# Kernel tuning notes

Hardware: AMD Instinct MI355X
Metric: run time of the kernel (lower is better)

## Reference

```python
import jax, jax.numpy as jnp
import numpy as np


def setup_inputs() -> dict:
    key = jax.random.key(0)
    ks = jax.random.split(key, 9)
    B, Nq, Nkv, C, ICO = 1, 512, 2562, 64, 64
    return {
        "q": jax.random.normal(ks[0], (B, Nq, C), jnp.float32),
        "q_coord": jax.random.normal(ks[1], (B, Nq, 3), jnp.float32),
        "kv": jax.random.normal(ks[2], (B, Nkv, ICO), jnp.float32),
        "kv_coord": jax.random.normal(ks[3], (B, Nkv, 3), jnp.float32),
        "Wq": jax.random.normal(ks[4], (C, C), jnp.float32) * (C ** -0.5),
        "Wkv": jax.random.normal(ks[5], (ICO, 2 * C), jnp.float32) * (ICO ** -0.5),
        "Wdelta": jax.random.normal(ks[6], (3, C), jnp.float32) * (3 ** -0.5),
        "Wproj": jax.random.normal(ks[7], (C, C), jnp.float32) * (C ** -0.5),
        "bproj": jnp.zeros((C,), jnp.float32),
    }


def reference(q, q_coord, kv, kv_coord, Wq, Wkv, Wdelta, Wproj, bproj):
    C = q.shape[-1]
    scale = 1.0 / C  # erp_dim ** -1 (qk_scale=None)
    q_ = q @ Wq                                   # [B, Nq, C]
    kv_ = kv @ Wkv                                # [B, Nkv, 2C]
    k, v = jnp.split(kv_, 2, axis=-1)             # each [B, Nkv, C]
    # positional encoding: exp(-|dq - dk|) over 3D coords, projected to C
    pos_enc = jnp.exp(-jnp.abs(q_coord[:, :, None] - kv_coord[:, None])) @ Wdelta  # [B,Nq,Nkv,C]
    # elementwise abs-diff attention score, reduced over channel dim
    score = (jnp.exp(-jnp.abs(q_[:, :, None] - k[:, None])) + pos_enc).sum(-1) * scale  # [B,Nq,Nkv]
    attn = jax.nn.softmax(score, axis=-1)
    out = attn @ v                                # [B, Nq, C]
    return out @ Wproj + bproj
```

## Files before the change

### kernel.cpp

```cpp
#include <hip/hip_runtime.h>

#define NQ   512
#define NKV  2562
#define CH   64
#define QB   2
#define BT   512
#define NJQ  4
#define JQ   641
#define PSTRIDE 132
#define LOG2E 1.44269504088896340736f

#define KVROWS 8
#define NKVB ((NKV + KVROWS - 1) / KVROWS)
#define QROWS 16
#define NQB (NQ / QROWS)
#define NCB  41

static __device__ __forceinline__ float exp2_raw(float x) {
  float r; asm("v_exp_f32 %0, %1" : "=v"(r) : "v"(x)); return r;
}
static __device__ __forceinline__ float exp2_negabs(float x) {
  float r; asm("v_exp_f32 %0, -abs(%1)" : "=v"(r) : "v"(x)); return r;
}
#define E2(a, b) exp2_negabs((a) - (b))

__global__ __launch_bounds__(256) void gemm_qkv(
    const float* __restrict__ q, const float* __restrict__ kv,
    const float* __restrict__ Wq, const float* __restrict__ Wkv,
    const float* __restrict__ kvc, float* __restrict__ qp,
    float* __restrict__ kvp, float* __restrict__ kvc4) {
  const int tid = threadIdx.x;
  if (blockIdx.x < NKVB) {
    const int j0 = blockIdx.x * KVROWS;
    __shared__ float s_in[KVROWS][CH];
    if (tid < KVROWS * (CH / 4)) {
      int r = tid >> 4, g = tid & 15;
      int j = j0 + r;
      float4 v = (j < NKV) ? ((const float4*)(kv + (size_t)j * CH))[g]
                           : make_float4(0.f, 0.f, 0.f, 0.f);
      ((float4*)&s_in[r][0])[g] = v;
    }
    __syncthreads();
    const int r = tid >> 5;
    const int mg = (tid & 31) * 4;
    float4 acc = make_float4(0.f, 0.f, 0.f, 0.f);
#pragma unroll 16
    for (int rr = 0; rr < CH; ++rr) {
      float a = s_in[r][rr];
      float4 w = *(const float4*)(Wkv + (size_t)rr * 2 * CH + mg);
      acc.x = fmaf(a, w.x, acc.x); acc.y = fmaf(a, w.y, acc.y);
      acc.z = fmaf(a, w.z, acc.z); acc.w = fmaf(a, w.w, acc.w);
    }
    if (mg < CH) {
      acc.x *= LOG2E; acc.y *= LOG2E; acc.z *= LOG2E; acc.w *= LOG2E;
    }
    int j = j0 + r;
    if (j < NKV) *(float4*)(kvp + (size_t)j * 2 * CH + mg) = acc;
  } else if (blockIdx.x < NKVB + NQB) {
    const int i0 = (blockIdx.x - NKVB) * QROWS;
    __shared__ float s_in[QROWS][CH];
    {
      int r = tid >> 4, g = tid & 15;
      float4 v = ((const float4*)(q + (size_t)(i0 + r) * CH))[g];
      ((float4*)&s_in[r][0])[g] = v;
    }
    __syncthreads();
    const int r = tid >> 4;
    const int cg = (tid & 15) * 4;
    float4 acc = make_float4(0.f, 0.f, 0.f, 0.f);
#pragma unroll 16
    for (int rr = 0; rr < CH; ++rr) {
      float a = s_in[r][rr];
      float4 w = *(const float4*)(Wq + (size_t)rr * CH + cg);
      acc.x = fmaf(a, w.x, acc.x); acc.y = fmaf(a, w.y, acc.y);
      acc.z = fmaf(a, w.z, acc.z); acc.w = fmaf(a, w.w, acc.w);
    }
    acc.x *= LOG2E; acc.y *= LOG2E; acc.z *= LOG2E; acc.w *= LOG2E;
    *(float4*)(qp + (size_t)(i0 + r) * CH + cg) = acc;
  } else {
    int t = (blockIdx.x - NKVB - NQB) * 256 + tid;
    if (t < NKV * 4) {
      int j = t >> 2, d = t & 3;
      kvc4[t] = (d < 3) ? kvc[(size_t)j * 3 + d] * LOG2E : 0.f;
    }
  }
}

__global__ __launch_bounds__(BT, 4) void attn_part(
    const float* __restrict__ qp, const float* __restrict__ kvp,
    const float* __restrict__ qc, const float* __restrict__ kvc4,
    const float* __restrict__ Wdelta, float* __restrict__ part) {
  __shared__ float s_score[QB][JQ];
  __shared__ float s_red[QB][BT];
  __shared__ float s_wd[3];

  const int qpair = blockIdx.x >> 2;
  const int h = blockIdx.x & 3;
  const int i0 = qpair * QB;
  const int jlo = h * JQ;
  const int jhi = (jlo + JQ < NKV) ? jlo + JQ : NKV;

  const int tid = threadIdx.x;
  const int sub = tid & 3;
  const int c0 = sub * 16;
  const int wid = tid >> 6;
  const int lane = tid & 63;

  if (tid < 3) {
    float s = 0.f;
    for (int c = 0; c < CH; ++c) s += Wdelta[tid * CH + c];
    s_wd[tid] = s;
  }

  const float4* q0p = (const float4*)(qp + (size_t)i0 * CH + c0);
  const float4* q1p = (const float4*)(qp + (size_t)(i0 + 1) * CH + c0);
  float4 qa0 = q0p[0], qa1 = q0p[1], qa2 = q0p[2], qa3 = q0p[3];
  float4 qb0 = q1p[0], qb1 = q1p[1], qb2 = q1p[2], qb3 = q1p[3];
  asm volatile("" : "+v"(qa0.x), "+v"(qa0.y), "+v"(qa0.z), "+v"(qa0.w),
                    "+v"(qa1.x), "+v"(qa1.y), "+v"(qa1.z), "+v"(qa1.w),
                    "+v"(qa2.x), "+v"(qa2.y), "+v"(qa2.z), "+v"(qa2.w),
                    "+v"(qa3.x), "+v"(qa3.y), "+v"(qa3.z), "+v"(qa3.w));
  asm volatile("" : "+v"(qb0.x), "+v"(qb0.y), "+v"(qb0.z), "+v"(qb0.w),
                    "+v"(qb1.x), "+v"(qb1.y), "+v"(qb1.z), "+v"(qb1.w),
                    "+v"(qb2.x), "+v"(qb2.y), "+v"(qb2.z), "+v"(qb2.w),
                    "+v"(qb3.x), "+v"(qb3.y), "+v"(qb3.z), "+v"(qb3.w));

  float qc0[3], qc1[3];
#pragma unroll
  for (int d = 0; d < 3; ++d) {
    qc0[d] = qc[(size_t)i0 * 3 + d] * LOG2E;
    qc1[d] = qc[(size_t)(i0 + 1) * 3 + d] * LOG2E;
  }
  __syncthreads();
  const float wd0 = s_wd[0], wd1 = s_wd[1], wd2 = s_wd[2];
  const float pscale = (1.0f / 64.0f) * LOG2E;

  const int step = BT / 4;
  float ls0 = 0.f, ls1 = 0.f;
  int j = jlo + (tid >> 2);
  float4 k0, k1, k2, k3, cc;
  {
    int jc = (j < jhi) ? j : jlo;
    const float4* kr = (const float4*)(kvp + (size_t)jc * 128 + c0);
    k0 = kr[0]; k1 = kr[1]; k2 = kr[2]; k3 = kr[3];
    cc = *(const float4*)(kvc4 + (size_t)jc * 4);
  }
  while (j < jhi) {
    const int jn = j + step;
    const int jnc = (jn < jhi) ? jn : jlo;
    const float4* krn = (const float4*)(kvp + (size_t)jnc * 128 + c0);
    float4 n0 = krn[0], n1 = krn[1], n2 = krn[2], n3 = krn[3];
    float4 cn = *(const float4*)(kvc4 + (size_t)jnc * 4);

    float s0 = ((E2(qa0.x, k0.x) + E2(qa0.y, k0.y)) + (E2(qa0.z, k0.z) + E2(qa0.w, k0.w)))
             + ((E2(qa1.x, k1.x) + E2(qa1.y, k1.y)) + (E2(qa1.z, k1.z) + E2(qa1.w, k1.w)))
             + ((E2(qa2.x, k2.x) + E2(qa2.y, k2.y)) + (E2(qa2.z, k2.z) + E2(qa2.w, k2.w)))
             + ((E2(qa3.x, k3.x) + E2(qa3.y, k3.y)) + (E2(qa3.z, k3.z) + E2(qa3.w, k3.w)));
    float s1 = ((E2(qb0.x, k0.x) + E2(qb0.y, k0.y)) + (E2(qb0.z, k0.z) + E2(qb0.w, k0.w)))
             + ((E2(qb1.x, k1.x) + E2(qb1.y, k1.y)) + (E2(qb1.z, k1.z) + E2(qb1.w, k1.w)))
             + ((E2(qb2.x, k2.x) + E2(qb2.y, k2.y)) + (E2(qb2.z, k2.z) + E2(qb2.w, k2.w)))
             + ((E2(qb3.x, k3.x) + E2(qb3.y, k3.y)) + (E2(qb3.z, k3.z) + E2(qb3.w, k3.w)));
    s0 += __shfl_xor(s0, 1); s0 += __shfl_xor(s0, 2);
    s1 += __shfl_xor(s1, 1); s1 += __shfl_xor(s1, 2);
    if (sub == 0) {
      s0 += E2(qc0[0], cc.x) * wd0 + E2(qc0[1], cc.y) * wd1 + E2(qc0[2], cc.z) * wd2;
      s1 += E2(qc1[0], cc.x) * wd0 + E2(qc1[1], cc.y) * wd1 + E2(qc1[2], cc.z) * wd2;
      float p0 = exp2_raw(s0 * pscale);
      float p1 = exp2_raw(s1 * pscale);
      s_score[0][j - jlo] = p0; s_score[1][j - jlo] = p1;
      ls0 += p0; ls1 += p1;
    }
    k0 = n0; k1 = n1; k2 = n2; k3 = n3; cc = cn;
    j = jn;
  }

#pragma unroll
  for (int off = 1; off < 64; off <<= 1) {
    ls0 += __shfl_xor(ls0, off);
    ls1 += __shfl_xor(ls1, off);
  }
  if (lane == 0) { s_red[0][wid] = ls0; s_red[1][wid] = ls1; }
  __syncthreads();
  float t0 = s_red[0][0], t1 = s_red[1][0];
#pragma unroll
  for (int w = 1; w < BT / 64; ++w) { t0 += s_red[0][w]; t1 += s_red[1][w]; }
  __syncthreads();

  const int c = tid & 63, g = tid >> 6;
  float a0 = 0.f, a1 = 0.f;
#pragma unroll 8
  for (int j2 = jlo + g; j2 < jhi; j2 += 8) {
    float v = kvp[(size_t)j2 * 128 + 64 + c];
    a0 = fmaf(s_score[0][j2 - jlo], v, a0);
    a1 = fmaf(s_score[1][j2 - jlo], v, a1);
  }
  s_red[0][tid] = a0; s_red[1][tid] = a1;
  __syncthreads();

  float* P = part + (size_t)(qpair * NJQ + h) * PSTRIDE;
  if (g == 0) {
    float u0 = 0.f, u1 = 0.f;
#pragma unroll
    for (int gg = 0; gg < 8; ++gg) {
      u0 += s_red[0][gg * 64 + c];
      u1 += s_red[1][gg * 64 + c];
    }
    P[4 + c] = u0;
    P[68 + c] = u1;
    if (c == 0) { P[0] = t0; P[1] = t1; }
  }
}

__global__ __launch_bounds__(256) void attn_merge(
    const float* __restrict__ part, const float* __restrict__ Wproj,
    const float* __restrict__ bproj, float* __restrict__ out) {
  __shared__ float s_o[4][CH];
  const int tid = threadIdx.x;
  const int g = tid >> 6, c = tid & 63;
  const int i = blockIdx.x * 4 + g;
  const int qpi = i >> 1, qs = i & 1;

  float ssum = 0.f, osum = 0.f;
#pragma unroll
  for (int h = 0; h < NJQ; ++h) {
    const float* P = part + (size_t)(qpi * NJQ + h) * PSTRIDE;
    ssum += P[qs];
    osum += P[4 + qs * 64 + c];
  }
  s_o[g][c] = osum / ssum;
  __syncthreads();

  float acc = 0.f;
#pragma unroll 16
  for (int r = 0; r < CH; ++r)
    acc = fmaf(s_o[g][r], Wproj[r * CH + c], acc);
  out[(size_t)i * CH + c] = acc + bproj[c];
}

extern "C" void kernel_launch(void* const* d_in, const int* in_sizes, int n_in,
                              void* d_out, int out_size, void* d_ws, size_t ws_size,
                              hipStream_t stream) {
  const float* q      = (const float*)d_in[0];
  const float* qc     = (const float*)d_in[1];
  const float* kv     = (const float*)d_in[2];
  const float* kvc    = (const float*)d_in[3];
  const float* Wq     = (const float*)d_in[4];
  const float* Wkv    = (const float*)d_in[5];
  const float* Wdelta = (const float*)d_in[6];
  const float* Wproj  = (const float*)d_in[7];
  const float* bproj  = (const float*)d_in[8];
  float* outp = (float*)d_out;

  float* qp   = (float*)d_ws;
  float* kvp  = qp + NQ * CH;
  float* part = kvp + (size_t)NKV * 2 * CH;
  float* kvc4 = part + (size_t)(NQ / QB) * NJQ * PSTRIDE;

  gemm_qkv<<<NKVB + NQB + NCB, 256, 0, stream>>>(q, kv, Wq, Wkv, kvc, qp, kvp, kvc4);
  attn_part<<<(NQ / QB) * NJQ, BT, 0, stream>>>(qp, kvp, qc, kvc4, Wdelta, part);
  attn_merge<<<NQ / 4, 256, 0, stream>>>(part, Wproj, bproj, outp);
}
```

Before: 106.5 us.

## Process four queries per block with smaller KV splits and drop prefetch

Each attention block now handles four query rows instead of two, so every loaded key row is reused across four score computations. Block size drops to 256 threads and the KV range is split eight ways instead of four, keeping the grid at 1024 blocks. The software prefetch of the next key row is removed in favour of a plain loop. The cost is more registers per thread (64 query values held live), which may lower occupancy, and memory latency is no longer hidden by explicit prefetch.

After: 102.8 us, median of 2. 3.4% less time.

```diff
diff --git a/kernel.cpp b/kernel.cpp
--- a/kernel.cpp
+++ b/kernel.cpp
@@ -3,11 +3,11 @@
 #define NQ   512
 #define NKV  2562
 #define CH   64
-#define QB   2
-#define BT   512
-#define NJQ  4
-#define JQ   641
-#define PSTRIDE 132
+#define QB   4
+#define BT   256
+#define NJQ  8
+#define JQ   321
+#define PSTRIDE 260
 #define LOG2E 1.44269504088896340736f
 
 #define KVROWS 8
@@ -23,6 +23,8 @@
   float r; asm("v_exp_f32 %0, -abs(%1)" : "=v"(r) : "v"(x)); return r;
 }
 #define E2(a, b) exp2_negabs((a) - (b))
+#define T4(qf, kf) ((E2((qf).x, (kf).x) + E2((qf).y, (kf).y)) + \
+                    (E2((qf).z, (kf).z) + E2((qf).w, (kf).w)))
 
 __global__ __launch_bounds__(256) void gemm_qkv(
     const float* __restrict__ q, const float* __restrict__ kv,
@@ -94,9 +96,9 @@
   __shared__ float s_red[QB][BT];
   __shared__ float s_wd[3];
 
-  const int qpair = blockIdx.x >> 2;
-  const int h = blockIdx.x & 3;
-  const int i0 = qpair * QB;
+  const int qquad = blockIdx.x >> 3;
+  const int h = blockIdx.x & 7;
+  const int i0 = qquad * QB;
   const int jlo = h * JQ;
   const int jhi = (jlo + JQ < NKV) ? jlo + JQ : NKV;
 
@@ -112,102 +114,127 @@
     s_wd[tid] = s;
   }
 
-  const float4* q0p = (const float4*)(qp + (size_t)i0 * CH + c0);
-  const float4* q1p = (const float4*)(qp + (size_t)(i0 + 1) * CH + c0);
-  float4 qa0 = q0p[0], qa1 = q0p[1], qa2 = q0p[2], qa3 = q0p[3];
-  float4 qb0 = q1p[0], qb1 = q1p[1], qb2 = q1p[2], qb3 = q1p[3];
-  asm volatile("" : "+v"(qa0.x), "+v"(qa0.y), "+v"(qa0.z), "+v"(qa0.w),
-                    "+v"(qa1.x), "+v"(qa1.y), "+v"(qa1.z), "+v"(qa1.w),
-                    "+v"(qa2.x), "+v"(qa2.y), "+v"(qa2.z), "+v"(qa2.w),
-                    "+v"(qa3.x), "+v"(qa3.y), "+v"(qa3.z), "+v"(qa3.w));
-  asm volatile("" : "+v"(qb0.x), "+v"(qb0.y), "+v"(qb0.z), "+v"(qb0.w),
-                    "+v"(qb1.x), "+v"(qb1.y), "+v"(qb1.z), "+v"(qb1.w),
-                    "+v"(qb2.x), "+v"(qb2.y), "+v"(qb2.z), "+v"(qb2.w),
-                    "+v"(qb3.x), "+v"(qb3.y), "+v"(qb3.z), "+v"(qb3.w));
-
-  float qc0[3], qc1[3];
-#pragma unroll
-  for (int d = 0; d < 3; ++d) {
-    qc0[d] = qc[(size_t)i0 * 3 + d] * LOG2E;
-    qc1[d] = qc[(size_t)(i0 + 1) * 3 + d] * LOG2E;
-  }
+  const float4* pw = (const float4*)(qp + (size_t)(i0 + 0) * CH + c0);
+  const float4* px = (const float4*)(qp + (size_t)(i0 + 1) * CH + c0);
+  const float4* py = (const float4*)(qp + (size_t)(i0 + 2) * CH + c0);
+  const float4* pz = (const float4*)(qp + (size_t)(i0 + 3) * CH + c0);
+  float4 qw0 = pw[0], qw1 = pw[1], qw2 = pw[2], qw3 = pw[3];
+  float4 qx0 = px[0], qx1 = px[1], qx2 = px[2], qx3 = px[3];
+  float4 qy0 = py[0], qy1 = py[1], qy2 = py[2], qy3 = py[3];
+  float4 qz0 = pz[0], qz1 = pz[1], qz2 = pz[2], qz3 = pz[3];
+  asm volatile("" : "+v"(qw0.x), "+v"(qw0.y), "+v"(qw0.z), "+v"(qw0.w),
+                    "+v"(qw1.x), "+v"(qw1.y), "+v"(qw1.z), "+v"(qw1.w),
+                    "+v"(qw2.x), "+v"(qw2.y), "+v"(qw2.z), "+v"(qw2.w),
+                    "+v"(qw3.x), "+v"(qw3.y), "+v"(qw3.z), "+v"(qw3.w));
+  asm volatile("" : "+v"(qx0.x), "+v"(qx0.y), "+v"(qx0.z), "+v"(qx0.w),
+                    "+v"(qx1.x), "+v"(qx1.y), "+v"(qx1.z), "+v"(qx1.w),
+                    "+v"(qx2.x), "+v"(qx2.y), "+v"(qx2.z), "+v"(qx2.w),
+                    "+v"(qx3.x), "+v"(qx3.y), "+v"(qx3.z), "+v"(qx3.w));
+  asm volatile("" : "+v"(qy0.x), "+v"(qy0.y), "+v"(qy0.z), "+v"(qy0.w),
+                    "+v"(qy1.x), "+v"(qy1.y), "+v"(qy1.z), "+v"(qy1.w),
+                    "+v"(qy2.x), "+v"(qy2.y), "+v"(qy2.z), "+v"(qy2.w),
+                    "+v"(qy3.x), "+v"(qy3.y), "+v"(qy3.z), "+v"(qy3.w));
+  asm volatile("" : "+v"(qz0.x), "+v"(qz0.y), "+v"(qz0.z), "+v"(qz0.w),
+                    "+v"(qz1.x), "+v"(qz1.y), "+v"(qz1.z), "+v"(qz1.w),
+                    "+v"(qz2.x), "+v"(qz2.y), "+v"(qz2.z), "+v"(qz2.w),
+                    "+v"(qz3.x), "+v"(qz3.y), "+v"(qz3.z), "+v"(qz3.w));
+
+  float cw0 = qc[(size_t)(i0 + 0) * 3 + 0] * LOG2E;
+  float cw1 = qc[(size_t)(i0 + 0) * 3 + 1] * LOG2E;
+  float cw2 = qc[(size_t)(i0 + 0) * 3 + 2] * LOG2E;
+  float cx0 = qc[(size_t)(i0 + 1) * 3 + 0] * LOG2E;
+  float cx1 = qc[(size_t)(i0 + 1) * 3 + 1] * LOG2E;
+  float cx2 = qc[(size_t)(i0 + 1) * 3 + 2] * LOG2E;
+  float cy0 = qc[(size_t)(i0 + 2) * 3 + 0] * LOG2E;
+  float cy1 = qc[(size_t)(i0 + 2) * 3 + 1] * LOG2E;
+  float cy2 = qc[(size_t)(i0 + 2) * 3 + 2] * LOG2E;
+  float cz0 = qc[(size_t)(i0 + 3) * 3 + 0] * LOG2E;
+  float cz1 = qc[(size_t)(i0 + 3) * 3 + 1] * LOG2E;
+  float cz2 = qc[(size_t)(i0 + 3) * 3 + 2] * LOG2E;
   __syncthreads();
   const float wd0 = s_wd[0], wd1 = s_wd[1], wd2 = s_wd[2];
   const float pscale = (1.0f / 64.0f) * LOG2E;
 
-  const int step = BT / 4;
-  float ls0 = 0.f, ls1 = 0.f;
-  int j = jlo + (tid >> 2);
-  float4 k0, k1, k2, k3, cc;
-  {
-    int jc = (j < jhi) ? j : jlo;
-    const float4* kr = (const float4*)(kvp + (size_t)jc * 128 + c0);
-    k0 = kr[0]; k1 = kr[1]; k2 = kr[2]; k3 = kr[3];
-    cc = *(const float4*)(kvc4 + (size_t)jc * 4);
-  }
-  while (j < jhi) {
-    const int jn = j + step;
-    const int jnc = (jn < jhi) ? jn : jlo;
-    const float4* krn = (const float4*)(kvp + (size_t)jnc * 128 + c0);
-    float4 n0 = krn[0], n1 = krn[1], n2 = krn[2], n3 = krn[3];
-    float4 cn = *(const float4*)(kvc4 + (size_t)jnc * 4);
-
-    float s0 = ((E2(qa0.x, k0.x) + E2(qa0.y, k0.y)) + (E2(qa0.z, k0.z) + E2(qa0.w, k0.w)))
-             + ((E2(qa1.x, k1.x) + E2(qa1.y, k1.y)) + (E2(qa1.z, k1.z) + E2(qa1.w, k1.w)))
-             + ((E2(qa2.x, k2.x) + E2(qa2.y, k2.y)) + (E2(qa2.z, k2.z) + E2(qa2.w, k2.w)))
-             + ((E2(qa3.x, k3.x) + E2(qa3.y, k3.y)) + (E2(qa3.z, k3.z) + E2(qa3.w, k3.w)));
-    float s1 = ((E2(qb0.x, k0.x) + E2(qb0.y, k0.y)) + (E2(qb0.z, k0.z) + E2(qb0.w, k0.w)))
-             + ((E2(qb1.x, k1.x) + E2(qb1.y, k1.y)) + (E2(qb1.z, k1.z) + E2(qb1.w, k1.w)))
-             + ((E2(qb2.x, k2.x) + E2(qb2.y, k2.y)) + (E2(qb2.z, k2.z) + E2(qb2.w, k2.w)))
-             + ((E2(qb3.x, k3.x) + E2(qb3.y, k3.y)) + (E2(qb3.z, k3.z) + E2(qb3.w, k3.w)));
-    s0 += __shfl_xor(s0, 1); s0 += __shfl_xor(s0, 2);
-    s1 += __shfl_xor(s1, 1); s1 += __shfl_xor(s1, 2);
+  float lsw = 0.f, lsx = 0.f, lsy = 0.f, lsz = 0.f;
+  for (int j = jlo + (tid >> 2); j < jhi; j += BT / 4) {
+    const float4* kr = (const float4*)(kvp + (size_t)j * 128 + c0);
+    float4 k0 = kr[0], k1 = kr[1], k2 = kr[2], k3 = kr[3];
+    float4 cc = *(const float4*)(kvc4 + (size_t)j * 4);
+
+    float sw = (T4(qw0, k0) + T4(qw1, k1)) + (T4(qw2, k2) + T4(qw3, k3));
+    float sx = (T4(qx0, k0) + T4(qx1, k1)) + (T4(qx2, k2) + T4(qx3, k3));
+    float sy = (T4(qy0, k0) + T4(qy1, k1)) + (T4(qy2, k2) + T4(qy3, k3));
+    float sz = (T4(qz0, k0) + T4(qz1, k1)) + (T4(qz2, k2) + T4(qz3, k3));
+    sw += __shfl_xor(sw, 1); sw += __shfl_xor(sw, 2);
+    sx += __shfl_xor(sx, 1); sx += __shfl_xor(sx, 2);
+    sy += __shfl_xor(sy, 1); sy += __shfl_xor(sy, 2);
+    sz += __shfl_xor(sz, 1); sz += __shfl_xor(sz, 2);
     if (sub == 0) {
-      s0 += E2(qc0[0], cc.x) * wd0 + E2(qc0[1], cc.y) * wd1 + E2(qc0[2], cc.z) * wd2;
-      s1 += E2(qc1[0], cc.x) * wd0 + E2(qc1[1], cc.y) * wd1 + E2(qc1[2], cc.z) * wd2;
-      float p0 = exp2_raw(s0 * pscale);
-      float p1 = exp2_raw(s1 * pscale);
-      s_score[0][j - jlo] = p0; s_score[1][j - jlo] = p1;
-      ls0 += p0; ls1 += p1;
-    }
-    k0 = n0; k1 = n1; k2 = n2; k3 = n3; cc = cn;
-    j = jn;
+      int jj = j - jlo;
+      sw += E2(cw0, cc.x) * wd0 + E2(cw1, cc.y) * wd1 + E2(cw2, cc.z) * wd2;
+      sx += E2(cx0, cc.x) * wd0 + E2(cx1, cc.y) * wd1 + E2(cx2, cc.z) * wd2;
+      sy += E2(cy0, cc.x) * wd0 + E2(cy1, cc.y) * wd1 + E2(cy2, cc.z) * wd2;
+      sz += E2(cz0, cc.x) * wd0 + E2(cz1, cc.y) * wd1 + E2(cz2, cc.z) * wd2;
+      float p0 = exp2_raw(sw * pscale);
+      float p1 = exp2_raw(sx * pscale);
+      float p2 = exp2_raw(sy * pscale);
+      float p3 = exp2_raw(sz * pscale);
+      s_score[0][jj] = p0; s_score[1][jj] = p1;
+      s_score[2][jj] = p2; s_score[3][jj] = p3;
+      lsw += p0; lsx += p1; lsy += p2; lsz += p3;
+    }
   }
 
 #pragma unroll
   for (int off = 1; off < 64; off <<= 1) {
-    ls0 += __shfl_xor(ls0, off);
-    ls1 += __shfl_xor(ls1, off);
-  }
-  if (lane == 0) { s_red[0][wid] = ls0; s_red[1][wid] = ls1; }
-  __syncthreads();
-  float t0 = s_red[0][0], t1 = s_red[1][0];
-#pragma unroll
-  for (int w = 1; w < BT / 64; ++w) { t0 += s_red[0][w]; t1 += s_red[1][w]; }
+    lsw += __shfl_xor(lsw, off);
+    lsx += __shfl_xor(lsx, off);
+    lsy += __shfl_xor(lsy, off);
+    lsz += __shfl_xor(lsz, off);
+  }
+  if (lane == 0) {
+    s_red[0][wid] = lsw; s_red[1][wid] = lsx;
+    s_red[2][wid] = lsy; s_red[3][wid] = lsz;
+  }
+  __syncthreads();
+  float tw = s_red[0][0], tx = s_red[1][0], ty = s_red[2][0], tz = s_red[3][0];
+#pragma unroll
+  for (int w = 1; w < BT / 64; ++w) {
+    tw += s_red[0][w]; tx += s_red[1][w];
+    ty += s_red[2][w]; tz += s_red[3][w];
+  }
   __syncthreads();
 
   const int c = tid & 63, g = tid >> 6;
-  float a0 = 0.f, a1 = 0.f;
+  float aw = 0.f, ax = 0.f, ay = 0.f, az = 0.f;
 #pragma unroll 8
-  for (int j2 = jlo + g; j2 < jhi; j2 += 8) {
+  for (int j2 = jlo + g; j2 < jhi; j2 += 4) {
     float v = kvp[(size_t)j2 * 128 + 64 + c];
-    a0 = fmaf(s_score[0][j2 - jlo], v, a0);
-    a1 = fmaf(s_score[1][j2 - jlo], v, a1);
-  }
-  s_red[0][tid] = a0; s_red[1][tid] = a1;
-  __syncthreads();
-
-  float* P = part + (size_t)(qpair * NJQ + h) * PSTRIDE;
+    int jj = j2 - jlo;
+    aw = fmaf(s_score[0][jj], v, aw);
+    ax = fmaf(s_score[1][jj], v, ax);
+    ay = fmaf(s_score[2][jj], v, ay);
+    az = fmaf(s_score[3][jj], v, az);
+  }
+  s_red[0][tid] = aw; s_red[1][tid] = ax;
+  s_red[2][tid] = ay; s_red[3][tid] = az;
+  __syncthreads();
+
+  float* P = part + (size_t)(qquad * NJQ + h) * PSTRIDE;
   if (g == 0) {
-    float u0 = 0.f, u1 = 0.f;
-#pragma unroll
-    for (int gg = 0; gg < 8; ++gg) {
-      u0 += s_red[0][gg * 64 + c];
-      u1 += s_red[1][gg * 64 + c];
-    }
-    P[4 + c] = u0;
-    P[68 + c] = u1;
-    if (c == 0) { P[0] = t0; P[1] = t1; }
+    float uw = 0.f, ux = 0.f, uy = 0.f, uz = 0.f;
+#pragma unroll
+    for (int gg = 0; gg < 4; ++gg) {
+      uw += s_red[0][gg * 64 + c];
+      ux += s_red[1][gg * 64 + c];
+      uy += s_red[2][gg * 64 + c];
+      uz += s_red[3][gg * 64 + c];
+    }
+    P[4 + 0 * 64 + c] = uw;
+    P[4 + 1 * 64 + c] = ux;
+    P[4 + 2 * 64 + c] = uy;
+    P[4 + 3 * 64 + c] = uz;
+    if (c == 0) { P[0] = tw; P[1] = tx; P[2] = ty; P[3] = tz; }
   }
 }
 
@@ -216,24 +243,24 @@
     const float* __restrict__ bproj, float* __restrict__ out) {
   __shared__ float s_o[4][CH];
   const int tid = threadIdx.x;
-  const int g = tid >> 6, c = tid & 63;
-  const int i = blockIdx.x * 4 + g;
-  const int qpi = i >> 1, qs = i & 1;
+  const int qs = tid >> 6, c = tid & 63;
+  const int qquad = blockIdx.x;
+  const int i = qquad * 4 + qs;
 
   float ssum = 0.f, osum = 0.f;
 #pragma unroll
   for (int h = 0; h < NJQ; ++h) {
-    const float* P = part + (size_t)(qpi * NJQ + h) * PSTRIDE;
+    const float* P = part + (size_t)(qquad * NJQ + h) * PSTRIDE;
     ssum += P[qs];
     osum += P[4 + qs * 64 + c];
   }
-  s_o[g][c] = osum / ssum;
+  s_o[qs][c] = osum / ssum;
   __syncthreads();
 
   float acc = 0.f;
 #pragma unroll 16
   for (int r = 0; r < CH; ++r)
-    acc = fmaf(s_o[g][r], Wproj[r * CH + c], acc);
+    acc = fmaf(s_o[qs][r], Wproj[r * CH + c], acc);
   out[(size_t)i * CH + c] = acc + bproj[c];
 }
 
@@ -258,5 +285,5 @@
 
   gemm_qkv<<<NKVB + NQB + NCB, 256, 0, stream>>>(q, kv, Wq, Wkv, kvc, qp, kvp, kvc4);
   attn_part<<<(NQ / QB) * NJQ, BT, 0, stream>>>(qp, kvp, qc, kvc4, Wdelta, part);
-  attn_merge<<<NQ / 4, 256, 0, stream>>>(part, Wproj, bproj, outp);
-}
+  attn_merge<<<NQ / QB, 256, 0, stream>>>(part, Wproj, bproj, outp);
+}
```
